# Kernel optimization log

Measured on AMD Instinct MI355X. Metric: run time of the kernel, lower is better.

The kernel has to match this reference:

```python
import jax, jax.numpy as jnp
import numpy as np

WS = 8          # window size -> N = 64
SHIFT = 4       # shift size for shifted windows
FEAT = 32       # feature map H = W at stage 3
C = 512         # channels (SwinV2-B stage 3)
HEADS = 16
B_IMG = 128     # images -> 128 * (32/8)^2 = 2048 windows


def _rel_coords_table():
    # log-spaced continuous relative coords table, SwinV2 style: [(2W-1)^2, 2]
    r = np.arange(-(WS - 1), WS, dtype=np.float32)
    t = np.stack(np.meshgrid(r, r, indexing='ij'), axis=-1)  # [15,15,2]
    t = t / (WS - 1) * 8.0
    t = np.sign(t) * np.log2(np.abs(t) + 1.0) / np.log2(8.0)
    return t.reshape(-1, 2)


def _rel_pos_index():
    c = np.stack(np.meshgrid(np.arange(WS), np.arange(WS), indexing='ij'))  # [2,8,8]
    cf = c.reshape(2, -1)
    rel = (cf[:, :, None] - cf[:, None, :]).transpose(1, 2, 0)  # [64,64,2]
    rel[:, :, 0] += WS - 1
    rel[:, :, 1] += WS - 1
    rel[:, :, 0] *= 2 * WS - 1
    return rel.sum(-1).astype(np.int32)  # [64,64]


def _shift_mask():
    # standard SwinV2 shifted-window attention mask: [nW, N, N] in {0, -100}
    img = np.zeros((FEAT, FEAT), dtype=np.float32)
    cnt = 0
    for hs in (slice(0, -WS), slice(-WS, -SHIFT), slice(-SHIFT, None)):
        for ws in (slice(0, -WS), slice(-WS, -SHIFT), slice(-SHIFT, None)):
            img[hs, ws] = cnt
            cnt += 1
    win = img.reshape(FEAT // WS, WS, FEAT // WS, WS).transpose(0, 2, 1, 3)
    win = win.reshape(-1, WS * WS)  # [nW, 64]
    diff = win[:, None, :] - win[:, :, None]
    return np.where(diff != 0, -100.0, 0.0).astype(np.float32)


def setup_inputs() -> dict:
    key = jax.random.key(0)
    ks = jax.random.split(key, 10)
    nW = (FEAT // WS) ** 2  # 16 windows per image
    Bw = B_IMG * nW         # 2048
    N = WS * WS
    s = 0.02
    return {
        'x': jax.random.normal(ks[0], (Bw, N, C), jnp.float32),
        'mask': jnp.asarray(_shift_mask()),
        'qkv_w': jax.random.normal(ks[1], (3 * C, C), jnp.float32) * s,
        'q_bias': jnp.zeros((C,), jnp.float32),
        'v_bias': jnp.zeros((C,), jnp.float32),
        'logit_scale': jnp.full((HEADS, 1, 1), np.log(10.0), jnp.float32),
        'cpb_w1': jax.random.normal(ks[2], (512, 2), jnp.float32) * s,
        'cpb_b1': jnp.zeros((512,), jnp.float32),
        'cpb_w2': jax.random.normal(ks[3], (HEADS, 512), jnp.float32) * s,
        'proj_w': jax.random.normal(ks[4], (C, C), jnp.float32) * s,
        'proj_b': jnp.zeros((C,), jnp.float32),
        'rel_coords_table': jnp.asarray(_rel_coords_table()),
        'rel_pos_index': jnp.asarray(_rel_pos_index()),
    }


def reference(x, mask, qkv_w, q_bias, v_bias, logit_scale, cpb_w1, cpb_b1,
              cpb_w2, proj_w, proj_b, rel_coords_table, rel_pos_index):
    Bw, N, Cdim = x.shape
    H = logit_scale.shape[0]
    d = Cdim // H
    # qkv projection; k has no bias (SwinV2)
    qkv_bias = jnp.concatenate([q_bias, jnp.zeros_like(q_bias), v_bias])
    qkv = (x @ qkv_w.T + qkv_bias).reshape(Bw, N, 3, H, d).transpose(2, 0, 3, 1, 4)
    q, k, v = qkv[0], qkv[1], qkv[2]  # each [Bw,H,N,d]
    # cosine attention with learned per-head temperature
    qn = q / jnp.maximum(jnp.linalg.norm(q, axis=-1, keepdims=True), 1e-12)
    kn = k / jnp.maximum(jnp.linalg.norm(k, axis=-1, keepdims=True), 1e-12)
    attn = jnp.einsum('bhnd,bhmd->bhnm', qn, kn)
    scale = jnp.exp(jnp.minimum(logit_scale, jnp.log(100.0)))  # [H,1,1]
    attn = attn * scale[None]
    # continuous relative position bias via small MLP over log-spaced coords
    tbl = jax.nn.relu(rel_coords_table @ cpb_w1.T + cpb_b1) @ cpb_w2.T  # [(2W-1)^2,H]
    bias = tbl[rel_pos_index.reshape(-1)].reshape(N, N, H).transpose(2, 0, 1)
    attn = attn + 16.0 * jax.nn.sigmoid(bias)[None]
    # shifted-window mask applied per window group
    nW = mask.shape[0]
    attn = attn.reshape(Bw // nW, nW, H, N, N) + mask[None, :, None]
    attn = jax.nn.softmax(attn.reshape(Bw, H, N, N), axis=-1)
    out = jnp.einsum('bhnm,bhmd->bhnd', attn, v)
    out = out.transpose(0, 2, 1, 3).reshape(Bw, N, Cdim)
    return out @ proj_w.T + proj_b
```

## Files before the change

### kernel.cpp

```cpp
#include <hip/hip_runtime.h>
#include <stdint.h>
#include <stddef.h>


typedef __attribute__((ext_vector_type(8))) short bf16x8;
typedef __attribute__((ext_vector_type(4))) float f32x4;
typedef __attribute__((ext_vector_type(4))) unsigned short us4;
typedef __attribute__((ext_vector_type(8))) unsigned short us8;
typedef unsigned short u16;
typedef unsigned int u32;

#define FENCE() asm volatile("" ::: "memory")
#define WAITV4() asm volatile("s_waitcnt vmcnt(4)" ::: "memory")
#define WAITV3() asm volatile("s_waitcnt vmcnt(3)" ::: "memory")
#define WAITV0() asm volatile("s_waitcnt vmcnt(0)" ::: "memory")
#define WAITL0() asm volatile("s_waitcnt lgkmcnt(0)" ::: "memory")

__device__ __forceinline__ u16 f2bf(float f) {
  union { __bf16 b; u16 u; } cv;
  cv.b = (__bf16)f;
  return cv.u;
}
__device__ __forceinline__ float bf2f(u16 s) {
  return __uint_as_float(((u32)s) << 16);
}
__device__ __forceinline__ void gl_lds16(const void* g, void* l) {
  __builtin_amdgcn_global_load_lds(
      (const __attribute__((address_space(1))) u32*)g,
      (__attribute__((address_space(3))) u32*)l, 16, 0, 0);
}
__device__ __forceinline__ f32x4 mfma16(bf16x8 a, bf16x8 b, f32x4 c) {
  return __builtin_amdgcn_mfma_f32_16x16x32_bf16(a, b, c, 0, 0, 0);
}
__device__ __forceinline__ bf16x8 ldswz(const u16* p, int ks) {
  return *(const bf16x8*)((const u16*)((uintptr_t)p ^ (uintptr_t)(ks << 6)));
}


__global__ void prep_kernel(const float* __restrict__ X, u16* __restrict__ XB,
                            const float* __restrict__ QW, const float* __restrict__ PW,
                            u16* __restrict__ WQB, u16* __restrict__ WPB,
                            const float* __restrict__ CT, const float* __restrict__ W1,
                            const float* __restrict__ B1, const float* __restrict__ W2,
                            float* __restrict__ SIG) {
  const int b = blockIdx.x, tid = threadIdx.x;
  if (b < 32768) {
    size_t idx = (size_t)b * 256 + tid;
    float4 a = ((const float4*)X)[idx * 2];
    float4 c = ((const float4*)X)[idx * 2 + 1];
    us8 o;
    o[0] = f2bf(a.x); o[1] = f2bf(a.y); o[2] = f2bf(a.z); o[3] = f2bf(a.w);
    o[4] = f2bf(c.x); o[5] = f2bf(c.y); o[6] = f2bf(c.z); o[7] = f2bf(c.w);
    *(us8*)&XB[idx * 8] = o;
  } else if (b < 33792) {
    int idx = (b - 32768) * 256 + tid;
    const int NQ = 1536 * 512 / 4;
    float4 v; u16* dst;
    if (idx < NQ) { v = ((const float4*)QW)[idx]; dst = WQB + (size_t)idx * 4; }
    else { int k = idx - NQ; v = ((const float4*)PW)[k]; dst = WPB + (size_t)k * 4; }
    us4 u; u.x = f2bf(v.x); u.y = f2bf(v.y); u.z = f2bf(v.z); u.w = f2bf(v.w);
    *(us4*)dst = u;
  } else {
    int i = b - 33792;
    float c0 = CT[i * 2 + 0], c1 = CT[i * 2 + 1];
    float a[16];
    #pragma unroll
    for (int hh = 0; hh < 16; ++hh) a[hh] = 0.f;
    #pragma unroll
    for (int jj = 0; jj < 2; ++jj) {
      int j = tid + jj * 256;
      float h = fmaxf(c0 * W1[j * 2 + 0] + c1 * W1[j * 2 + 1] + B1[j], 0.f);
      #pragma unroll
      for (int hh = 0; hh < 16; ++hh) a[hh] += h * W2[hh * 512 + j];
    }
    __shared__ float red[4][16];
    #pragma unroll
    for (int hh = 0; hh < 16; ++hh) {
      float v = a[hh];
      for (int m = 1; m < 64; m <<= 1) v += __shfl_xor(v, m);
      if ((tid & 63) == 0) red[tid >> 6][hh] = v;
    }
    __syncthreads();
    if (tid < 16) {
      float v = red[0][tid] + red[1][tid] + red[2][tid] + red[3][tid];
      SIG[i * 16 + tid] = 16.f / (1.f + __expf(-v));
    }
  }
}


#define GEMM32_KLOOP()                                                     \
  _Pragma("unroll")                                                        \
  for (int t = 0; t < 16; ++t) {                                           \
    const int Sb = (t % 3) * 12288;                                        \
    _Pragma("unroll")                                                      \
    for (int m = 0; m < 4; ++m)                                            \
      af[m] = *(const bf16x8*)&S[Sb + (wm * 64 + m * 16 + fr) * 32 + fsw]; \
    _Pragma("unroll")                                                      \
    for (int n = 0; n < 2; ++n)                                            \
      bf[n] = *(const bf16x8*)&S[Sb + 4096 + (wn * 64 + n * 16 + fr) * 32 + fsw]; \
    if (t + 2 <= 15) stageB(t + 2);                                        \
    FENCE(); __builtin_amdgcn_s_barrier(); FENCE();                        \
    WAITL0(); __builtin_amdgcn_sched_barrier(0);                           \
    __builtin_amdgcn_s_setprio(1);                                         \
    _Pragma("unroll")                                                      \
    for (int m = 0; m < 4; ++m)                                            \
      _Pragma("unroll")                                                    \
      for (int n = 0; n < 2; ++n)                                          \
        acc[m][n] = mfma16(af[m], bf[n], acc[m][n]);                       \
    __builtin_amdgcn_s_setprio(0);                                         \
    FENCE(); __builtin_amdgcn_s_barrier(); FENCE();                        \
    _Pragma("unroll")                                                      \
    for (int n = 0; n < 2; ++n)                                            \
      bf[n] = *(const bf16x8*)&S[Sb + 4096 + (wn * 64 + (n + 2) * 16 + fr) * 32 + fsw]; \
    if (t + 3 <= 15) stageA(t + 3);                                        \
    if (t <= 12) { WAITV4(); }                                             \
    else if (t == 13) { WAITV3(); }                                        \
    else if (t == 14) { WAITV0(); }                                        \
    FENCE(); __builtin_amdgcn_s_barrier(); FENCE();                        \
    WAITL0(); __builtin_amdgcn_sched_barrier(0);                           \
    __builtin_amdgcn_s_setprio(1);                                         \
    _Pragma("unroll")                                                      \
    for (int m = 0; m < 4; ++m)                                            \
      _Pragma("unroll")                                                    \
      for (int n = 0; n < 2; ++n)                                          \
        acc[m][n + 2] = mfma16(af[m], bf[n], acc[m][n + 2]);               \
    __builtin_amdgcn_s_setprio(0);                                         \
    FENCE(); __builtin_amdgcn_s_barrier(); FENCE();                        \
  }


__global__ __launch_bounds__(512, 4) void qkv_g32(
    const u16* __restrict__ XB, const u16* __restrict__ WB,
    const float* __restrict__ QB, const float* __restrict__ VB,
    u16* __restrict__ QKV,
    const float* __restrict__ SIG, const float* __restrict__ MASK,
    const int* __restrict__ RPI, float* __restrict__ CMB) {
  __shared__ u16 S[36864];
  const int tid = threadIdx.x, lane = tid & 63, w = tid >> 6;
  int bid = blockIdx.x;
  if (bid >= 6144) {
    int b2 = bid - 6144;
    int mw = b2 >> 4, h = b2 & 15;
    const float* mrow = &MASK[(size_t)mw * 4096];
    float* crow = &CMB[(size_t)b2 * 4096];
    #pragma unroll
    for (int it = 0; it < 8; ++it) {
      int nm = it * 512 + tid;
      crow[nm] = SIG[RPI[nm] * 16 + h] + mrow[nm];
    }
    return;
  }
  int swz = (bid & 7) * 768 + (bid >> 3);
  const int mt = swz / 6, nt = swz - mt * 6;
  const long m0 = (long)mt * 128, n0 = (long)nt * 256;
  const int wm = w >> 2, wn = w & 3;
  const int fr = lane & 15, lg = lane >> 4;
  const int fsw = (lg ^ ((fr >> 1) & 3)) << 3;
  const f32x4 zf = {0.f, 0.f, 0.f, 0.f};

  f32x4 acc[4][4];
  #pragma unroll
  for (int mi = 0; mi < 4; ++mi)
    #pragma unroll
    for (int ni = 0; ni < 4; ++ni) acc[mi][ni] = zf;

  const int arow = tid >> 2;
  const int asc = (tid & 3) ^ ((arow >> 1) & 3);
  const u16* aSrc = &XB[(size_t)(m0 + arow) * 512 + asc * 8];
  const u16* bSrc0 = &WB[(size_t)(n0 + arow) * 512 + asc * 8];
  const u16* bSrc1 = &WB[(size_t)(n0 + 128 + arow) * 512 + asc * 8];

  auto stageA = [&](int kt) {
    gl_lds16(aSrc + kt * 32, &S[(kt % 3) * 12288 + w * 512]);
  };
  auto stageB = [&](int kt) {
    gl_lds16(bSrc0 + kt * 32, &S[(kt % 3) * 12288 + 4096 + w * 512]);
    gl_lds16(bSrc1 + kt * 32, &S[(kt % 3) * 12288 + 8192 + w * 512]);
  };

  bf16x8 af[4], bf[2];

  stageA(0); stageB(0); stageA(1); stageB(1); stageA(2);
  WAITV4();
  FENCE(); __builtin_amdgcn_s_barrier(); FENCE();

  GEMM32_KLOOP()

  u16* eb = &S[w * 4608];
  #pragma unroll
  for (int ni = 0; ni < 4; ++ni) {
    const long c = n0 + wn * 64 + ni * 16 + fr;
    float bias = (c < 512) ? QB[c] : (c < 1024 ? 0.f : VB[c - 1024]);
    #pragma unroll
    for (int mi = 0; mi < 4; ++mi)
      #pragma unroll
      for (int r = 0; r < 4; ++r)
        eb[(mi * 16 + lg * 4 + r) * 72 + ni * 16 + fr] = f2bf(acc[mi][ni][r] + bias);
  }
  WAITL0();
  #pragma unroll
  for (int i = 0; i < 8; ++i) {
    int row = i * 8 + (lane >> 3);
    int c16 = lane & 7;
    us8 v = *(const us8*)&eb[row * 72 + c16 * 8];
    *(us8*)&QKV[(size_t)(m0 + wm * 64 + row) * 1536 + n0 + wn * 64 + c16 * 8] = v;
  }
}


__global__ __launch_bounds__(512, 4) void proj_g32(
    const u16* __restrict__ A, const u16* __restrict__ WB,
    const float* __restrict__ PB, float* __restrict__ OUT) {
  __shared__ u16 S[36864];
  const int tid = threadIdx.x, lane = tid & 63, w = tid >> 6;
  int bid = blockIdx.x;
  int swz = (bid & 7) * 256 + (bid >> 3);
  const int mt = swz >> 1, nt = swz & 1;
  const long m0 = (long)mt * 128, n0 = (long)nt * 256;
  const int wm = w >> 2, wn = w & 3;
  const int fr = lane & 15, lg = lane >> 4;
  const int fsw = (lg ^ ((fr >> 1) & 3)) << 3;
  const f32x4 zf = {0.f, 0.f, 0.f, 0.f};

  f32x4 acc[4][4];
  #pragma unroll
  for (int mi = 0; mi < 4; ++mi)
    #pragma unroll
    for (int ni = 0; ni < 4; ++ni) acc[mi][ni] = zf;

  const int arow = tid >> 2;
  const int asc = (tid & 3) ^ ((arow >> 1) & 3);
  const u16* aSrc = &A[(size_t)(m0 + arow) * 1536 + asc * 8];
  const u16* bSrc0 = &WB[(size_t)(n0 + arow) * 512 + asc * 8];
  const u16* bSrc1 = &WB[(size_t)(n0 + 128 + arow) * 512 + asc * 8];

  auto stageA = [&](int kt) {
    gl_lds16(aSrc + kt * 32, &S[(kt % 3) * 12288 + w * 512]);
  };
  auto stageB = [&](int kt) {
    gl_lds16(bSrc0 + kt * 32, &S[(kt % 3) * 12288 + 4096 + w * 512]);
    gl_lds16(bSrc1 + kt * 32, &S[(kt % 3) * 12288 + 8192 + w * 512]);
  };

  bf16x8 af[4], bf[2];

  stageA(0); stageB(0); stageA(1); stageB(1); stageA(2);
  WAITV4();
  FENCE(); __builtin_amdgcn_s_barrier(); FENCE();

  GEMM32_KLOOP()

  #pragma unroll
  for (int ni = 0; ni < 4; ++ni) {
    const long c = n0 + wn * 64 + ni * 16 + fr;
    float bias = PB[c];
    #pragma unroll
    for (int mi = 0; mi < 4; ++mi)
      #pragma unroll
      for (int r = 0; r < 4; ++r) {
        long row = m0 + wm * 64 + mi * 16 + lg * 4 + r;
        OUT[row * 512 + c] = acc[mi][ni][r] + bias;
      }
  }
}


__global__ __launch_bounds__(256, 2) void qkv_gemm_rs(
    const float* __restrict__ X, const u16* __restrict__ WB,
    const float* __restrict__ QB, const float* __restrict__ VB,
    u16* __restrict__ QKV) {
  __shared__ u16 As[128 * 64];
  __shared__ u16 Bs[128 * 64];
  const int tid = threadIdx.x, lane = tid & 63, w = tid >> 6;
  int bid = blockIdx.x;
  int swz = (bid & 7) * 1536 + (bid >> 3);
  const int mt = swz / 12, nt = swz - mt * 12;
  const long m0 = (long)mt * 128, n0 = (long)nt * 128;
  const int wm = w >> 1, wn = w & 1;
  const f32x4 zf = {0.f, 0.f, 0.f, 0.f};

  f32x4 acc[4][4];
  #pragma unroll
  for (int mi = 0; mi < 4; ++mi)
    #pragma unroll
    for (int ni = 0; ni < 4; ++ni) acc[mi][ni] = zf;

  const int fr = lane & 15;
  const int fsw = ((lane >> 4) ^ (lane & 7)) * 8;
  const u16* Ap = &As[(wm * 64 + fr) * 64 + fsw];
  const u16* Bp = &Bs[(wn * 64 + fr) * 64 + fsw];

  for (int t = 0; t < 8; ++t) {
    float4 av[8];
    #pragma unroll
    for (int i = 0; i < 8; ++i) {
      int ch = tid + (i << 8);
      int row = ch >> 4, kc = ch & 15;
      av[i] = *(const float4*)&X[(m0 + row) * 512 + t * 64 + kc * 4];
    }
    #pragma unroll
    for (int i = 0; i < 4; ++i) {
      int ch = ((w << 2) + i) * 64 + lane;
      int row = ch >> 3, kc = (ch & 7) ^ (row & 7);
      gl_lds16(&WB[(n0 + row) * 512 + t * 64 + kc * 8], &Bs[((w << 2) + i) * 512]);
    }
    #pragma unroll
    for (int i = 0; i < 8; ++i) {
      int ch = tid + (i << 8);
      int row = ch >> 4, kc = ch & 15;
      int kcs = kc ^ ((row & 7) << 1);
      us4 u; u.x = f2bf(av[i].x); u.y = f2bf(av[i].y); u.z = f2bf(av[i].z); u.w = f2bf(av[i].w);
      *(us4*)&As[row * 64 + kcs * 4] = u;
    }
    __syncthreads();
    #pragma unroll
    for (int ks = 0; ks < 2; ++ks) {
      bf16x8 af[4], bfr[4];
      #pragma unroll
      for (int mi = 0; mi < 4; ++mi) af[mi] = ldswz(Ap + mi * 1024, ks);
      #pragma unroll
      for (int ni = 0; ni < 4; ++ni) bfr[ni] = ldswz(Bp + ni * 1024, ks);
      #pragma unroll
      for (int mi = 0; mi < 4; ++mi)
        #pragma unroll
        for (int ni = 0; ni < 4; ++ni)
          acc[mi][ni] = mfma16(af[mi], bfr[ni], acc[mi][ni]);
    }
    __syncthreads();
  }

  #pragma unroll
  for (int ni = 0; ni < 4; ++ni) {
    const long c = n0 + wn * 64 + ni * 16 + (lane & 15);
    float bias = (c < 512) ? QB[c] : (c < 1024 ? 0.f : VB[c - 1024]);
    #pragma unroll
    for (int mi = 0; mi < 4; ++mi)
      #pragma unroll
      for (int r = 0; r < 4; ++r) {
        long row = m0 + wm * 64 + mi * 16 + (lane >> 4) * 4 + r;
        QKV[row * 1536 + c] = f2bf(acc[mi][ni][r] + bias);
      }
  }
}

__global__ void cmb_kernel(const float* __restrict__ SIG, const float* __restrict__ MASK,
                           const int* __restrict__ RPI, float* __restrict__ CMB) {
  int b = blockIdx.x;
  int w = b >> 4, h = b & 15;
  int tid = threadIdx.x;
  const float* mrow = &MASK[(size_t)w * 4096];
  float* crow = &CMB[(size_t)b * 4096];
  #pragma unroll
  for (int it = 0; it < 16; ++it) {
    int nm = it * 256 + tid;
    crow[nm] = SIG[RPI[nm] * 16 + h] + mrow[nm];
  }
}


__global__ __launch_bounds__(256, 3) void attn_wh(
    u16* __restrict__ QKV, const float* __restrict__ CMB, const float* __restrict__ LS) {
  __shared__ u16 smu[26112];
  const int tid = threadIdx.x, lane = tid & 63, w = tid >> 6;
  const int b = blockIdx.x;
  const int win = b >> 2;
  const int h = (b & 3) * 4 + w;
  const int wi = win & 15;
  const size_t base = (size_t)win * 64 * 1536;
  const int fr = lane & 15, lg = lane >> 4;
  u16* ps = &smu[w * 6528];
  u16* vt = ps + 4352;
  const float scale = __expf(fminf(LS[h], 4.6051702f));
  const float* cp = &CMB[((size_t)(wi * 16 + h)) << 12];
  const f32x4 zf = {0.f, 0.f, 0.f, 0.f};

  us8 vrow[4];
  #pragma unroll
  for (int c = 0; c < 4; ++c)
    vrow[c] = *(const us8*)&QKV[base + (size_t)lane * 1536 + 1024 + h * 32 + c * 8];

  f32x4 acc[4][4];
  #pragma unroll
  for (int m = 0; m < 4; ++m)
    #pragma unroll
    for (int n = 0; n < 4; ++n)
      #pragma unroll
      for (int r = 0; r < 4; ++r)
        acc[m][n][r] = cp[(m * 16 + lg * 4 + r) * 64 + n * 16 + fr];

  bf16x8 af[4], bk[4];
  #pragma unroll
  for (int m = 0; m < 4; ++m) {
    us8 qv = *(const us8*)&QKV[base + (size_t)(m * 16 + fr) * 1536 + h * 32 + lg * 8];
    float qf[8]; float ss = 0.f;
    #pragma unroll
    for (int j = 0; j < 8; ++j) { qf[j] = bf2f(qv[j]); ss += qf[j] * qf[j]; }
    ss += __shfl_xor(ss, 16); ss += __shfl_xor(ss, 32);
    float rn = scale / fmaxf(sqrtf(ss), 1e-12f);
    union { us8 u; bf16x8 b; } cv;
    #pragma unroll
    for (int j = 0; j < 8; ++j) cv.u[j] = f2bf(qf[j] * rn);
    af[m] = cv.b;
  }
  #pragma unroll
  for (int m = 0; m < 4; ++m) {
    us8 kv = *(const us8*)&QKV[base + (size_t)(m * 16 + fr) * 1536 + 512 + h * 32 + lg * 8];
    float kf[8]; float ss = 0.f;
    #pragma unroll
    for (int j = 0; j < 8; ++j) { kf[j] = bf2f(kv[j]); ss += kf[j] * kf[j]; }
    ss += __shfl_xor(ss, 16); ss += __shfl_xor(ss, 32);
    float rn = 1.f / fmaxf(sqrtf(ss), 1e-12f);
    union { us8 u; bf16x8 b; } cv;
    #pragma unroll
    for (int j = 0; j < 8; ++j) cv.u[j] = f2bf(kf[j] * rn);
    bk[m] = cv.b;
  }

  #pragma unroll
  for (int m = 0; m < 4; ++m)
    #pragma unroll
    for (int n = 0; n < 4; ++n)
      acc[m][n] = mfma16(af[m], bk[n], acc[m][n]);

  #pragma unroll
  for (int c = 0; c < 4; ++c)
    #pragma unroll
    for (int j = 0; j < 8; ++j)
      vt[(c * 8 + j) * 68 + lane] = vrow[c][j];

  #pragma unroll
  for (int m = 0; m < 4; ++m)
    #pragma unroll
    for (int r = 0; r < 4; ++r) {
      float pv[4];
      float mx = -3.0e38f;
      #pragma unroll
      for (int n = 0; n < 4; ++n) { pv[n] = acc[m][n][r]; mx = fmaxf(mx, pv[n]); }
      mx = fmaxf(mx, __shfl_xor(mx, 1));
      mx = fmaxf(mx, __shfl_xor(mx, 2));
      mx = fmaxf(mx, __shfl_xor(mx, 4));
      mx = fmaxf(mx, __shfl_xor(mx, 8));
      float sum = 0.f;
      #pragma unroll
      for (int n = 0; n < 4; ++n) { pv[n] = __expf(pv[n] - mx); sum += pv[n]; }
      sum += __shfl_xor(sum, 1); sum += __shfl_xor(sum, 2);
      sum += __shfl_xor(sum, 4); sum += __shfl_xor(sum, 8);
      float inv = 1.f / sum;
      #pragma unroll
      for (int n = 0; n < 4; ++n)
        ps[(m * 16 + lg * 4 + r) * 68 + n * 16 + fr] = f2bf(pv[n] * inv);
    }

  WAITL0(); __builtin_amdgcn_sched_barrier(0);

  f32x4 o[4][2];
  #pragma unroll
  for (int m = 0; m < 4; ++m) { o[m][0] = zf; o[m][1] = zf; }
  #pragma unroll
  for (int m = 0; m < 4; ++m)
    #pragma unroll
    for (int ks = 0; ks < 2; ++ks) {
      bf16x8 ap = *(const bf16x8*)&ps[(m * 16 + fr) * 68 + ks * 32 + lg * 8];
      #pragma unroll
      for (int n2 = 0; n2 < 2; ++n2) {
        bf16x8 bv = *(const bf16x8*)&vt[(n2 * 16 + fr) * 68 + ks * 32 + lg * 8];
        o[m][n2] = mfma16(ap, bv, o[m][n2]);
      }
    }

  #pragma unroll
  for (int m = 0; m < 4; ++m)
    #pragma unroll
    for (int n2 = 0; n2 < 2; ++n2)
      #pragma unroll
      for (int r = 0; r < 4; ++r)
        QKV[base + (size_t)(m * 16 + lg * 4 + r) * 1536 + h * 32 + n2 * 16 + fr] =
            f2bf(o[m][n2][r]);
}


extern "C" void kernel_launch(void* const* d_in, const int* in_sizes, int n_in,
                              void* d_out, int out_size, void* d_ws, size_t ws_size,
                              hipStream_t stream) {
  const float* X    = (const float*)d_in[0];
  const float* MASK = (const float*)d_in[1];
  const float* QW   = (const float*)d_in[2];
  const float* QB   = (const float*)d_in[3];
  const float* VB   = (const float*)d_in[4];
  const float* LS   = (const float*)d_in[5];
  const float* CW1  = (const float*)d_in[6];
  const float* CB1  = (const float*)d_in[7];
  const float* CW2  = (const float*)d_in[8];
  const float* PW   = (const float*)d_in[9];
  const float* PB   = (const float*)d_in[10];
  const float* CT   = (const float*)d_in[11];
  const int*   RPI  = (const int*)d_in[12];
  float* OUT = (float*)d_out;

  char* ws = (char*)d_ws;
  const bool big = ws_size >= 543178752ull;
  u16* QKV = (u16*)ws;
  u16* XB  = (u16*)(ws + 402653184ull);
  size_t off = big ? 536870912ull : 402653184ull;
  float* CMB = (float*)(ws + off);  off += 4194304ull;
  float* SIG = (float*)(ws + off);  off += 16384ull;
  u16*   WQB = (u16*)(ws + off);    off += 1572864ull;
  u16*   WPB = (u16*)(ws + off);

  if (big) {
    prep_kernel<<<34017, 256, 0, stream>>>(X, XB, QW, PW, WQB, WPB,
                                           CT, CW1, CB1, CW2, SIG);
    qkv_g32<<<6400, 512, 0, stream>>>(XB, WQB, QB, VB, QKV, SIG, MASK, RPI, CMB);
  } else {
    prep_kernel<<<34017, 256, 0, stream>>>(X, XB, QW, PW, WQB, WPB,
                                           CT, CW1, CB1, CW2, SIG);
    cmb_kernel<<<256, 256, 0, stream>>>(SIG, MASK, RPI, CMB);
    qkv_gemm_rs<<<12288, 256, 0, stream>>>(X, WQB, QB, VB, QKV);
  }
  attn_wh<<<8192, 256, 0, stream>>>(QKV, CMB, LS);
  proj_g32<<<2048, 512, 0, stream>>>(QKV, WPB, PB, OUT);
}
```

Before: 633.1 us.

## Shrink QKV GEMM LDS to double buffer to raise occupancy

The QKV projection GEMM moves from a three-stage LDS ring (72 KB) to a two-stage double buffer (48 KB) and raises the launch bound from 4 to 6 blocks per CU. The epilogue is split into two halves so the staging area fits in the smaller LDS. The aim is more resident waves to hide memory latency, but each k-step now waits for all outstanding loads (vmcnt 0), so there is less prefetch depth within a block.

```diff
diff --git a/kernel.cpp b/kernel.cpp
--- a/kernel.cpp
+++ b/kernel.cpp
@@ -85,6 +85,125 @@
       float v = red[0][tid] + red[1][tid] + red[2][tid] + red[3][tid];
       SIG[i * 16 + tid] = 16.f / (1.f + __expf(-v));
     }
+  }
+}
+
+
+__global__ __launch_bounds__(512, 6) void qkv_g32(
+    const u16* __restrict__ XB, const u16* __restrict__ WB,
+    const float* __restrict__ QB, const float* __restrict__ VB,
+    u16* __restrict__ QKV,
+    const float* __restrict__ SIG, const float* __restrict__ MASK,
+    const int* __restrict__ RPI, float* __restrict__ CMB) {
+  __shared__ u16 S[24576];
+  const int tid = threadIdx.x, lane = tid & 63, w = tid >> 6;
+  int bid = blockIdx.x;
+  if (bid >= 6144) {
+    int b2 = bid - 6144;
+    int mw = b2 >> 4, h = b2 & 15;
+    const float* mrow = &MASK[(size_t)mw * 4096];
+    float* crow = &CMB[(size_t)b2 * 4096];
+    #pragma unroll
+    for (int it = 0; it < 8; ++it) {
+      int nm = it * 512 + tid;
+      crow[nm] = SIG[RPI[nm] * 16 + h] + mrow[nm];
+    }
+    return;
+  }
+  int swz = (bid & 7) * 768 + (bid >> 3);
+  const int mt = swz / 6, nt = swz - mt * 6;
+  const long m0 = (long)mt * 128, n0 = (long)nt * 256;
+  const int wm = w >> 2, wn = w & 3;
+  const int fr = lane & 15, lg = lane >> 4;
+  const int fsw = (lg ^ ((fr >> 1) & 3)) << 3;
+  const f32x4 zf = {0.f, 0.f, 0.f, 0.f};
+
+  f32x4 acc[4][4];
+  #pragma unroll
+  for (int mi = 0; mi < 4; ++mi)
+    #pragma unroll
+    for (int ni = 0; ni < 4; ++ni) acc[mi][ni] = zf;
+
+  const int arow = tid >> 2;
+  const int asc = (tid & 3) ^ ((arow >> 1) & 3);
+  const u16* aSrc = &XB[(size_t)(m0 + arow) * 512 + asc * 8];
+  const u16* bSrc0 = &WB[(size_t)(n0 + arow) * 512 + asc * 8];
+  const u16* bSrc1 = &WB[(size_t)(n0 + 128 + arow) * 512 + asc * 8];
+
+  auto stageT = [&](int kt) {
+    int dst = (kt & 1) * 12288;
+    gl_lds16(aSrc + kt * 32, &S[dst + w * 512]);
+    gl_lds16(bSrc0 + kt * 32, &S[dst + 4096 + w * 512]);
+    gl_lds16(bSrc1 + kt * 32, &S[dst + 8192 + w * 512]);
+  };
+
+  bf16x8 af[4], bf[2];
+
+  stageT(0);
+  WAITV0();
+  FENCE(); __builtin_amdgcn_s_barrier(); FENCE();
+
+  #pragma unroll
+  for (int t = 0; t < 16; ++t) {
+    const int Sb = (t & 1) * 12288;
+    #pragma unroll
+    for (int m = 0; m < 4; ++m)
+      af[m] = *(const bf16x8*)&S[Sb + (wm * 64 + m * 16 + fr) * 32 + fsw];
+    #pragma unroll
+    for (int n = 0; n < 2; ++n)
+      bf[n] = *(const bf16x8*)&S[Sb + 4096 + (wn * 64 + n * 16 + fr) * 32 + fsw];
+    if (t + 1 <= 15) stageT(t + 1);
+    FENCE(); __builtin_amdgcn_s_barrier(); FENCE();
+    WAITL0(); __builtin_amdgcn_sched_barrier(0);
+    __builtin_amdgcn_s_setprio(1);
+    #pragma unroll
+    for (int m = 0; m < 4; ++m)
+      #pragma unroll
+      for (int n = 0; n < 2; ++n)
+        acc[m][n] = mfma16(af[m], bf[n], acc[m][n]);
+    __builtin_amdgcn_s_setprio(0);
+    FENCE(); __builtin_amdgcn_s_barrier(); FENCE();
+    #pragma unroll
+    for (int n = 0; n < 2; ++n)
+      bf[n] = *(const bf16x8*)&S[Sb + 4096 + (wn * 64 + (n + 2) * 16 + fr) * 32 + fsw];
+    if (t + 1 <= 15) { WAITV0(); }
+    FENCE(); __builtin_amdgcn_s_barrier(); FENCE();
+    WAITL0(); __builtin_amdgcn_sched_barrier(0);
+    __builtin_amdgcn_s_setprio(1);
+    #pragma unroll
+    for (int m = 0; m < 4; ++m)
+      #pragma unroll
+      for (int n = 0; n < 2; ++n)
+        acc[m][n + 2] = mfma16(af[m], bf[n], acc[m][n + 2]);
+    __builtin_amdgcn_s_setprio(0);
+    FENCE(); __builtin_amdgcn_s_barrier(); FENCE();
+  }
+
+  u16* eb = &S[w * 2304];
+  #pragma unroll
+  for (int half = 0; half < 2; ++half) {
+    #pragma unroll
+    for (int ni = 0; ni < 4; ++ni) {
+      const long c = n0 + wn * 64 + ni * 16 + fr;
+      float bias = (c < 512) ? QB[c] : (c < 1024 ? 0.f : VB[c - 1024]);
+      #pragma unroll
+      for (int mm = 0; mm < 2; ++mm) {
+        const int mi = half * 2 + mm;
+        #pragma unroll
+        for (int r = 0; r < 4; ++r)
+          eb[(mm * 16 + lg * 4 + r) * 72 + ni * 16 + fr] = f2bf(acc[mi][ni][r] + bias);
+      }
+    }
+    WAITL0(); __builtin_amdgcn_sched_barrier(0);
+    #pragma unroll
+    for (int j = 0; j < 4; ++j) {
+      int unit = j * 64 + lane;
+      int row32 = unit >> 3, c16 = unit & 7;
+      us8 v = *(const us8*)&eb[row32 * 72 + c16 * 8];
+      *(us8*)&QKV[(size_t)(m0 + wm * 64 + half * 32 + row32) * 1536 +
+                  n0 + wn * 64 + c16 * 8] = v;
+    }
+    WAITL0(); __builtin_amdgcn_sched_barrier(0);
   }
 }
 
@@ -130,85 +249,6 @@
   }
 
 
-__global__ __launch_bounds__(512, 4) void qkv_g32(
-    const u16* __restrict__ XB, const u16* __restrict__ WB,
-    const float* __restrict__ QB, const float* __restrict__ VB,
-    u16* __restrict__ QKV,
-    const float* __restrict__ SIG, const float* __restrict__ MASK,
-    const int* __restrict__ RPI, float* __restrict__ CMB) {
-  __shared__ u16 S[36864];
-  const int tid = threadIdx.x, lane = tid & 63, w = tid >> 6;
-  int bid = blockIdx.x;
-  if (bid >= 6144) {
-    int b2 = bid - 6144;
-    int mw = b2 >> 4, h = b2 & 15;
-    const float* mrow = &MASK[(size_t)mw * 4096];
-    float* crow = &CMB[(size_t)b2 * 4096];
-    #pragma unroll
-    for (int it = 0; it < 8; ++it) {
-      int nm = it * 512 + tid;
-      crow[nm] = SIG[RPI[nm] * 16 + h] + mrow[nm];
-    }
-    return;
-  }
-  int swz = (bid & 7) * 768 + (bid >> 3);
-  const int mt = swz / 6, nt = swz - mt * 6;
-  const long m0 = (long)mt * 128, n0 = (long)nt * 256;
-  const int wm = w >> 2, wn = w & 3;
-  const int fr = lane & 15, lg = lane >> 4;
-  const int fsw = (lg ^ ((fr >> 1) & 3)) << 3;
-  const f32x4 zf = {0.f, 0.f, 0.f, 0.f};
-
-  f32x4 acc[4][4];
-  #pragma unroll
-  for (int mi = 0; mi < 4; ++mi)
-    #pragma unroll
-    for (int ni = 0; ni < 4; ++ni) acc[mi][ni] = zf;
-
-  const int arow = tid >> 2;
-  const int asc = (tid & 3) ^ ((arow >> 1) & 3);
-  const u16* aSrc = &XB[(size_t)(m0 + arow) * 512 + asc * 8];
-  const u16* bSrc0 = &WB[(size_t)(n0 + arow) * 512 + asc * 8];
-  const u16* bSrc1 = &WB[(size_t)(n0 + 128 + arow) * 512 + asc * 8];
-
-  auto stageA = [&](int kt) {
-    gl_lds16(aSrc + kt * 32, &S[(kt % 3) * 12288 + w * 512]);
-  };
-  auto stageB = [&](int kt) {
-    gl_lds16(bSrc0 + kt * 32, &S[(kt % 3) * 12288 + 4096 + w * 512]);
-    gl_lds16(bSrc1 + kt * 32, &S[(kt % 3) * 12288 + 8192 + w * 512]);
-  };
-
-  bf16x8 af[4], bf[2];
-
-  stageA(0); stageB(0); stageA(1); stageB(1); stageA(2);
-  WAITV4();
-  FENCE(); __builtin_amdgcn_s_barrier(); FENCE();
-
-  GEMM32_KLOOP()
-
-  u16* eb = &S[w * 4608];
-  #pragma unroll
-  for (int ni = 0; ni < 4; ++ni) {
-    const long c = n0 + wn * 64 + ni * 16 + fr;
-    float bias = (c < 512) ? QB[c] : (c < 1024 ? 0.f : VB[c - 1024]);
-    #pragma unroll
-    for (int mi = 0; mi < 4; ++mi)
-      #pragma unroll
-      for (int r = 0; r < 4; ++r)
-        eb[(mi * 16 + lg * 4 + r) * 72 + ni * 16 + fr] = f2bf(acc[mi][ni][r] + bias);
-  }
-  WAITL0();
-  #pragma unroll
-  for (int i = 0; i < 8; ++i) {
-    int row = i * 8 + (lane >> 3);
-    int c16 = lane & 7;
-    us8 v = *(const us8*)&eb[row * 72 + c16 * 8];
-    *(us8*)&QKV[(size_t)(m0 + wm * 64 + row) * 1536 + n0 + wn * 64 + c16 * 8] = v;
-  }
-}
-
-
 __global__ __launch_bounds__(512, 4) void proj_g32(
     const u16* __restrict__ A, const u16* __restrict__ WB,
     const float* __restrict__ PB, float* __restrict__ OUT) {
```

Result: slower. 2.108 ms (+233.0%).
